# Kernel optimization log

Hardware: AMD Instinct MI355X
Metric: run time of the kernel (lower is better)

The kernel has to match this reference:

```python
import jax, jax.numpy as jnp
import numpy as np

WIN = 3  # win_size from init


def setup_inputs() -> dict:
    key = jax.random.key(0)
    ks = jax.random.split(key, 7)
    B, H, W, d = 8, 128, 128, 128
    N = H * W
    s = d ** -0.5  # param init scale
    return {
        "x": jax.random.normal(ks[0], (B, N, d), dtype=jnp.float32),
        "Wq": jax.random.normal(ks[1], (d, d), dtype=jnp.float32) * s,
        "bq": jax.random.normal(ks[2], (d,), dtype=jnp.float32) * 0.01,
        "Wk": jax.random.normal(ks[3], (d, d), dtype=jnp.float32) * s,
        "bk": jax.random.normal(ks[4], (d,), dtype=jnp.float32) * 0.01,
        "Wv": jax.random.normal(ks[5], (d, d), dtype=jnp.float32) * s,
        "bv": jax.random.normal(ks[6], (d,), dtype=jnp.float32) * 0.01,
        "H": H,
        "W": W,
    }


def reference(x, Wq, bq, Wk, bk, Wv, bv, H, W):
    B, N, d = x.shape
    scale = d ** -0.5
    pad = WIN // 2

    q = (x @ Wq + bq).reshape(B, H, W, d)
    k = (x @ Wk + bk).reshape(B, H, W, d)
    v = (x @ Wv + bv).reshape(B, H, W, d)

    # zero-pad spatial dims (matches F.pad); padded neighbors get logit 0, not -inf
    k_pad = jnp.pad(k, ((0, 0), (pad, pad), (pad, pad), (0, 0)))
    v_pad = jnp.pad(v, ((0, 0), (pad, pad), (pad, pad), (0, 0)))

    scores_l, vs_l = [], []
    for dy in range(WIN):
        for dx in range(WIN):
            k_slice = k_pad[:, dy:dy + H, dx:dx + W]   # [B,H,W,d]
            v_slice = v_pad[:, dy:dy + H, dx:dx + W]
            scores_l.append(jnp.einsum("bhwd,bhwd->bhw", q, k_slice) * scale)
            vs_l.append(v_slice)

    scores = jnp.stack(scores_l, axis=-1)            # [B,H,W,9]
    prob = jax.nn.softmax(scores, axis=-1)           # [B,H,W,9]
    v_stk = jnp.stack(vs_l, axis=-1)                 # [B,H,W,d,9]
    out = jnp.einsum("bhwn,bhwdn->bhwd", prob, v_stk)
    return out.reshape(B, N, d)
```

## Files before the change

kernel.cpp:

```cpp
#include <hip/hip_runtime.h>
#include <stdint.h>

#define B_ 8
#define H_ 128
#define W_ 128
#define D_ 128
#define N_ (H_*W_)
#define M_ (B_*N_)

typedef __attribute__((ext_vector_type(8))) short short8;
typedef __attribute__((ext_vector_type(4))) float floatx4;

typedef const __attribute__((address_space(1))) void* gas_t;
typedef __attribute__((address_space(3))) void* las_t;

__device__ inline unsigned short f2bf(float f){
  union { float f; unsigned int i; } c; c.f = f;
  unsigned int x = c.i;
  x += 0x7FFF + ((x >> 16) & 1);
  return (unsigned short)(x >> 16);
}
__device__ inline float bflo(unsigned int u){
  union { unsigned int i; float f; } c; c.i = u << 16; return c.f;
}
__device__ inline float bfhi(unsigned int u){
  union { unsigned int i; float f; } c; c.i = u & 0xFFFF0000u; return c.f;
}

__global__ void wtrans_kernel(const float* __restrict__ Wq, const float* __restrict__ Wk,
                              const float* __restrict__ Wv, unsigned short* __restrict__ Wt){
  const float* src = blockIdx.x == 0 ? Wq : (blockIdx.x == 1 ? Wk : Wv);
  unsigned short* dst = Wt + blockIdx.x * (D_*D_);
  const int i = blockIdx.y * 256 + threadIdx.x;
  const int k = i >> 7, n = i & 127;
  dst[n*D_ + k] = f2bf(src[i]);
}

__global__ __launch_bounds__(256, 2) void qkv_gemm_kernel(
    const float* __restrict__ x, const unsigned short* __restrict__ Wt,
    const float* __restrict__ bq, const float* __restrict__ bk, const float* __restrict__ bv,
    unsigned short* __restrict__ Q, unsigned short* __restrict__ K, unsigned short* __restrict__ V)
{
  const int which = blockIdx.x;
  const int rowTile = blockIdx.y;
  const float* bias = which == 0 ? bq : (which == 1 ? bk : bv);
  unsigned short* Out = which == 0 ? Q : (which == 1 ? K : V);
  const unsigned short* Wsel = Wt + which * (D_*D_);

  __shared__ unsigned short lds[32768];

  const int t = threadIdx.x;
  const int wave = t >> 6, lane = t & 63;

  {
    #pragma unroll
    for (int p = 0; p < 8; ++p){
      int s = p*256 + t;
      int n = s >> 4, cp = s & 15, c = cp ^ (n & 7);
      const unsigned short* gp = Wsel + n*128 + c*8;
      unsigned short* lp = (unsigned short*)lds + 16384 + p*2048 + wave*512;
      __builtin_amdgcn_global_load_lds((gas_t)(const void*)gp, (las_t)(void*)lp, 16, 0, 0);
    }
  }
  {
    const float* xrow = x + (size_t)rowTile * 128 * D_;
    #pragma unroll
    for (int p = 0; p < 8; ++p){
      int s = p*256 + t;
      int r = s >> 4, cp = s & 15, c = cp ^ (r & 7);
      const float* gp = xrow + r*D_ + c*8;
      float4 f0 = *(const float4*)gp;
      float4 f1 = *(const float4*)(gp + 4);
      uint4 pk;
      pk.x = (unsigned)f2bf(f0.x) | ((unsigned)f2bf(f0.y) << 16);
      pk.y = (unsigned)f2bf(f0.z) | ((unsigned)f2bf(f0.w) << 16);
      pk.z = (unsigned)f2bf(f1.x) | ((unsigned)f2bf(f1.y) << 16);
      pk.w = (unsigned)f2bf(f1.z) | ((unsigned)f2bf(f1.w) << 16);
      *(uint4*)&lds[s*8] = pk;
    }
  }
  __syncthreads();

  const int wm = (wave >> 1) * 64, wn = (wave & 1) * 64;
  const int m0 = lane & 15, quad = lane >> 4;

  floatx4 acc[4][4] = {};
  #pragma unroll
  for (int kk = 0; kk < 4; ++kk){
    short8 a[4], b[4];
    #pragma unroll
    for (int i = 0; i < 4; ++i){
      int row = wm + i*16 + m0;
      int c = (kk*4 + quad) ^ (row & 7);
      a[i] = *(const short8*)&lds[row*128 + c*8];
    }
    #pragma unroll
    for (int j = 0; j < 4; ++j){
      int n = wn + j*16 + m0;
      int c = (kk*4 + quad) ^ (n & 7);
      b[j] = *(const short8*)&lds[16384 + n*128 + c*8];
    }
    #pragma unroll
    for (int i = 0; i < 4; ++i)
      #pragma unroll
      for (int j = 0; j < 4; ++j)
        acc[i][j] = __builtin_amdgcn_mfma_f32_16x16x32_bf16(a[i], b[j], acc[i][j], 0, 0, 0);
  }

  __syncthreads();
  #pragma unroll
  for (int j = 0; j < 4; ++j){
    const int col = wn + j*16 + m0;
    const float bb = bias[col];
    #pragma unroll
    for (int i = 0; i < 4; ++i){
      #pragma unroll
      for (int r = 0; r < 4; ++r){
        int row = wm + i*16 + quad*4 + r;
        lds[row*136 + col] = f2bf(acc[i][j][r] + bb);
      }
    }
  }
  __syncthreads();
  unsigned short* Outp = Out + (size_t)rowTile * 128 * D_;
  #pragma unroll
  for (int p = 0; p < 8; ++p){
    int rr = p*16 + (t >> 4), cc = t & 15;
    uint4 v = *(const uint4*)&lds[rr*136 + cc*8];
    *(uint4*)(Outp + p*2048 + t*8) = v;
  }
}

__global__ __launch_bounds__(256) void attn_kernel(
    const unsigned short* __restrict__ Q, const unsigned short* __restrict__ K,
    const unsigned short* __restrict__ V, float* __restrict__ out)
{
  const int t = threadIdx.x;
  const int quarter = t & 3;
  const int pix = blockIdx.x * 64 + (t >> 2);
  const int w = pix & 127;
  const int h = (pix >> 7) & 127;
  const float scale = 0.08838834764831845f;

  const size_t off = (size_t)pix * D_ + quarter * 32;

  float q[32];
  {
    const unsigned short* qp = Q + off;
    #pragma unroll
    for (int c = 0; c < 4; ++c){
      uint4 u = *(const uint4*)(qp + c*8);
      unsigned uu[4] = {u.x, u.y, u.z, u.w};
      #pragma unroll
      for (int e = 0; e < 4; ++e){
        q[c*8 + e*2]     = bflo(uu[e]) * scale;
        q[c*8 + e*2 + 1] = bfhi(uu[e]) * scale;
      }
    }
  }

  float s[9];
  #pragma unroll
  for (int i = 0; i < 9; ++i){
    const int dy = i/3 - 1, dx = i%3 - 1;
    const bool ok = ((unsigned)(h + dy) < 128u) && ((unsigned)(w + dx) < 128u);
    float acc = 0.f;
    if (ok){
      const unsigned short* kp = K + off + (dy*W_ + dx) * D_;
      #pragma unroll
      for (int c = 0; c < 4; ++c){
        uint4 u = *(const uint4*)(kp + c*8);
        unsigned uu[4] = {u.x, u.y, u.z, u.w};
        #pragma unroll
        for (int e = 0; e < 4; ++e){
          acc += q[c*8 + e*2]     * bflo(uu[e]);
          acc += q[c*8 + e*2 + 1] * bfhi(uu[e]);
        }
      }
    }
    s[i] = acc;
  }
  #pragma unroll
  for (int i = 0; i < 9; ++i){
    s[i] += __shfl_xor(s[i], 1, 64);
    s[i] += __shfl_xor(s[i], 2, 64);
  }

  float m = s[0];
  #pragma unroll
  for (int i = 1; i < 9; ++i) m = fmaxf(m, s[i]);
  float p[9]; float l = 0.f;
  #pragma unroll
  for (int i = 0; i < 9; ++i){ p[i] = __expf(s[i] - m); l += p[i]; }
  const float inv = 1.f / l;

  float o[32];
  #pragma unroll
  for (int d = 0; d < 32; ++d) o[d] = 0.f;
  #pragma unroll
  for (int i = 0; i < 9; ++i){
    const int dy = i/3 - 1, dx = i%3 - 1;
    const bool ok = ((unsigned)(h + dy) < 128u) && ((unsigned)(w + dx) < 128u);
    if (ok){
      const float pi = p[i];
      const unsigned short* vp = V + off + (dy*W_ + dx) * D_;
      #pragma unroll
      for (int c = 0; c < 4; ++c){
        uint4 u = *(const uint4*)(vp + c*8);
        unsigned uu[4] = {u.x, u.y, u.z, u.w};
        #pragma unroll
        for (int e = 0; e < 4; ++e){
          o[c*8 + e*2]     += pi * bflo(uu[e]);
          o[c*8 + e*2 + 1] += pi * bfhi(uu[e]);
        }
      }
    }
  }

  float* op = out + off;
  #pragma unroll
  for (int c = 0; c < 8; ++c){
    float4 v4 = make_float4(o[c*4]*inv, o[c*4+1]*inv, o[c*4+2]*inv, o[c*4+3]*inv);
    *(float4*)(op + c*4) = v4;
  }
}

extern "C" void kernel_launch(void* const* d_in, const int* in_sizes, int n_in,
                              void* d_out, int out_size, void* d_ws, size_t ws_size,
                              hipStream_t stream)
{
  const float* x  = (const float*)d_in[0];
  const float* Wq = (const float*)d_in[1];
  const float* bq = (const float*)d_in[2];
  const float* Wk = (const float*)d_in[3];
  const float* bk = (const float*)d_in[4];
  const float* Wv = (const float*)d_in[5];
  const float* bv = (const float*)d_in[6];
  float* out = (float*)d_out;

  char* ws = (char*)d_ws;
  unsigned short* Wt = (unsigned short*)ws;
  unsigned short* Q  = (unsigned short*)(ws + (1<<17));
  unsigned short* K  = (unsigned short*)(ws + (1<<17) + (size_t)M_*D_*2);
  unsigned short* V  = (unsigned short*)(ws + (1<<17) + (size_t)2*M_*D_*2);

  hipLaunchKernelGGL(wtrans_kernel, dim3(3, 64), dim3(256), 0, stream, Wq, Wk, Wv, Wt);
  hipLaunchKernelGGL(qkv_gemm_kernel, dim3(3, M_/128), dim3(256), 0, stream,
                     x, Wt, bq, bk, bv, Q, K, V);
  hipLaunchKernelGGL(attn_kernel, dim3(M_/64), dim3(256), 0, stream, Q, K, V, out);
}
```

Baseline: 222.3 us.

## Reuse converted x tile across Q/K/V in GEMM; batch neighbor loads in attention

The QKV GEMM now launches one block per 128-row tile and loops over the three projections. The fp32 x tile is loaded and converted to bf16 once instead of three times, and the epilogue is staged in two halves to fit LDS. The attention kernel splits each pixel across 8 lanes of 16 channels instead of 4 lanes of 32, and issues all nine K and V neighbor loads up front into registers to raise memory-level parallelism. The trade-off is fewer, longer GEMM blocks with more barriers, and higher register pressure in attention under the new launch bound.

New measurement: 260.4 us. 17.1% more time.

```diff
diff --git a/kernel.cpp b/kernel.cpp
--- a/kernel.cpp
+++ b/kernel.cpp
@@ -41,27 +41,13 @@
     const float* __restrict__ bq, const float* __restrict__ bk, const float* __restrict__ bv,
     unsigned short* __restrict__ Q, unsigned short* __restrict__ K, unsigned short* __restrict__ V)
 {
-  const int which = blockIdx.x;
-  const int rowTile = blockIdx.y;
-  const float* bias = which == 0 ? bq : (which == 1 ? bk : bv);
-  unsigned short* Out = which == 0 ? Q : (which == 1 ? K : V);
-  const unsigned short* Wsel = Wt + which * (D_*D_);
+  const int rowTile = blockIdx.x;
 
   __shared__ unsigned short lds[32768];
 
   const int t = threadIdx.x;
   const int wave = t >> 6, lane = t & 63;
 
-  {
-    #pragma unroll
-    for (int p = 0; p < 8; ++p){
-      int s = p*256 + t;
-      int n = s >> 4, cp = s & 15, c = cp ^ (n & 7);
-      const unsigned short* gp = Wsel + n*128 + c*8;
-      unsigned short* lp = (unsigned short*)lds + 16384 + p*2048 + wave*512;
-      __builtin_amdgcn_global_load_lds((gas_t)(const void*)gp, (las_t)(void*)lp, 16, 0, 0);
-    }
-  }
   {
     const float* xrow = x + (size_t)rowTile * 128 * D_;
     #pragma unroll
@@ -79,147 +65,182 @@
       *(uint4*)&lds[s*8] = pk;
     }
   }
-  __syncthreads();
 
   const int wm = (wave >> 1) * 64, wn = (wave & 1) * 64;
   const int m0 = lane & 15, quad = lane >> 4;
 
-  floatx4 acc[4][4] = {};
-  #pragma unroll
-  for (int kk = 0; kk < 4; ++kk){
-    short8 a[4], b[4];
-    #pragma unroll
-    for (int i = 0; i < 4; ++i){
-      int row = wm + i*16 + m0;
-      int c = (kk*4 + quad) ^ (row & 7);
-      a[i] = *(const short8*)&lds[row*128 + c*8];
-    }
-    #pragma unroll
-    for (int j = 0; j < 4; ++j){
-      int n = wn + j*16 + m0;
-      int c = (kk*4 + quad) ^ (n & 7);
-      b[j] = *(const short8*)&lds[16384 + n*128 + c*8];
-    }
-    #pragma unroll
-    for (int i = 0; i < 4; ++i)
-      #pragma unroll
-      for (int j = 0; j < 4; ++j)
-        acc[i][j] = __builtin_amdgcn_mfma_f32_16x16x32_bf16(a[i], b[j], acc[i][j], 0, 0, 0);
-  }
-
-  __syncthreads();
-  #pragma unroll
-  for (int j = 0; j < 4; ++j){
-    const int col = wn + j*16 + m0;
-    const float bb = bias[col];
-    #pragma unroll
-    for (int i = 0; i < 4; ++i){
-      #pragma unroll
-      for (int r = 0; r < 4; ++r){
-        int row = wm + i*16 + quad*4 + r;
-        lds[row*136 + col] = f2bf(acc[i][j][r] + bb);
-      }
-    }
-  }
-  __syncthreads();
-  unsigned short* Outp = Out + (size_t)rowTile * 128 * D_;
-  #pragma unroll
-  for (int p = 0; p < 8; ++p){
-    int rr = p*16 + (t >> 4), cc = t & 15;
-    uint4 v = *(const uint4*)&lds[rr*136 + cc*8];
-    *(uint4*)(Outp + p*2048 + t*8) = v;
-  }
-}
-
-__global__ __launch_bounds__(256) void attn_kernel(
+  #pragma unroll
+  for (int which = 0; which < 3; ++which){
+    const float* bias = which == 0 ? bq : (which == 1 ? bk : bv);
+    unsigned short* Out = which == 0 ? Q : (which == 1 ? K : V);
+    const unsigned short* Wsel = Wt + which * (D_*D_);
+
+    #pragma unroll
+    for (int p = 0; p < 8; ++p){
+      int s = p*256 + t;
+      int n = s >> 4, cp = s & 15, c = cp ^ (n & 7);
+      const unsigned short* gp = Wsel + n*128 + c*8;
+      unsigned short* lp = (unsigned short*)lds + 16384 + p*2048 + wave*512;
+      __builtin_amdgcn_global_load_lds((gas_t)(const void*)gp, (las_t)(void*)lp, 16, 0, 0);
+    }
+    __syncthreads();
+
+    floatx4 acc[4][4] = {};
+    #pragma unroll
+    for (int kk = 0; kk < 4; ++kk){
+      short8 a[4], b[4];
+      #pragma unroll
+      for (int i = 0; i < 4; ++i){
+        int row = wm + i*16 + m0;
+        int c = (kk*4 + quad) ^ (row & 7);
+        a[i] = *(const short8*)&lds[row*128 + c*8];
+      }
+      #pragma unroll
+      for (int j = 0; j < 4; ++j){
+        int n = wn + j*16 + m0;
+        int c = (kk*4 + quad) ^ (n & 7);
+        b[j] = *(const short8*)&lds[16384 + n*128 + c*8];
+      }
+      #pragma unroll
+      for (int i = 0; i < 4; ++i)
+        #pragma unroll
+        for (int j = 0; j < 4; ++j)
+          acc[i][j] = __builtin_amdgcn_mfma_f32_16x16x32_bf16(a[i], b[j], acc[i][j], 0, 0, 0);
+    }
+
+    __syncthreads();
+    unsigned short* Outp = Out + (size_t)rowTile * 128 * D_;
+    #pragma unroll
+    for (int half = 0; half < 2; ++half){
+      if ((wave >> 1) == half){
+        #pragma unroll
+        for (int j = 0; j < 4; ++j){
+          const int col = wn + j*16 + m0;
+          const float bb = bias[col];
+          #pragma unroll
+          for (int i = 0; i < 4; ++i){
+            #pragma unroll
+            for (int r = 0; r < 4; ++r){
+              int lrow = i*16 + quad*4 + r;
+              lds[16384 + lrow*136 + col] = f2bf(acc[i][j][r] + bb);
+            }
+          }
+        }
+      }
+      __syncthreads();
+      #pragma unroll
+      for (int p = 0; p < 4; ++p){
+        int rr = p*16 + (t >> 4), cc = t & 15;
+        uint4 vv = *(const uint4*)&lds[16384 + rr*136 + cc*8];
+        *(uint4*)(Outp + half*8192 + p*2048 + t*8) = vv;
+      }
+      __syncthreads();
+    }
+  }
+}
+
+__global__ __launch_bounds__(256, 4) void attn_kernel(
     const unsigned short* __restrict__ Q, const unsigned short* __restrict__ K,
     const unsigned short* __restrict__ V, float* __restrict__ out)
 {
   const int t = threadIdx.x;
-  const int quarter = t & 3;
-  const int pix = blockIdx.x * 64 + (t >> 2);
+  const int e8 = t & 7;
+  const int pix = blockIdx.x * 32 + (t >> 3);
   const int w = pix & 127;
   const int h = (pix >> 7) & 127;
   const float scale = 0.08838834764831845f;
 
-  const size_t off = (size_t)pix * D_ + quarter * 32;
-
-  float q[32];
+  const size_t off = (size_t)pix * D_ + e8 * 16;
+
+  float q[16];
   {
     const unsigned short* qp = Q + off;
-    #pragma unroll
-    for (int c = 0; c < 4; ++c){
-      uint4 u = *(const uint4*)(qp + c*8);
-      unsigned uu[4] = {u.x, u.y, u.z, u.w};
-      #pragma unroll
-      for (int e = 0; e < 4; ++e){
-        q[c*8 + e*2]     = bflo(uu[e]) * scale;
-        q[c*8 + e*2 + 1] = bfhi(uu[e]) * scale;
-      }
-    }
-  }
-
-  float s[9];
-  #pragma unroll
-  for (int i = 0; i < 9; ++i){
-    const int dy = i/3 - 1, dx = i%3 - 1;
-    const bool ok = ((unsigned)(h + dy) < 128u) && ((unsigned)(w + dx) < 128u);
-    float acc = 0.f;
-    if (ok){
-      const unsigned short* kp = K + off + (dy*W_ + dx) * D_;
-      #pragma unroll
-      for (int c = 0; c < 4; ++c){
-        uint4 u = *(const uint4*)(kp + c*8);
-        unsigned uu[4] = {u.x, u.y, u.z, u.w};
-        #pragma unroll
-        for (int e = 0; e < 4; ++e){
-          acc += q[c*8 + e*2]     * bflo(uu[e]);
-          acc += q[c*8 + e*2 + 1] * bfhi(uu[e]);
-        }
-      }
-    }
-    s[i] = acc;
-  }
-  #pragma unroll
-  for (int i = 0; i < 9; ++i){
-    s[i] += __shfl_xor(s[i], 1, 64);
-    s[i] += __shfl_xor(s[i], 2, 64);
-  }
-
-  float m = s[0];
-  #pragma unroll
-  for (int i = 1; i < 9; ++i) m = fmaxf(m, s[i]);
-  float p[9]; float l = 0.f;
-  #pragma unroll
-  for (int i = 0; i < 9; ++i){ p[i] = __expf(s[i] - m); l += p[i]; }
-  const float inv = 1.f / l;
-
-  float o[32];
-  #pragma unroll
-  for (int d = 0; d < 32; ++d) o[d] = 0.f;
+    uint4 u0 = *(const uint4*)qp;
+    uint4 u1 = *(const uint4*)(qp + 8);
+    unsigned uu[8] = {u0.x, u0.y, u0.z, u0.w, u1.x, u1.y, u1.z, u1.w};
+    #pragma unroll
+    for (int e = 0; e < 8; ++e){
+      q[e*2]     = bflo(uu[e]) * scale;
+      q[e*2 + 1] = bfhi(uu[e]) * scale;
+    }
+  }
+
+  uint4 ku[9][2];
   #pragma unroll
   for (int i = 0; i < 9; ++i){
     const int dy = i/3 - 1, dx = i%3 - 1;
     const bool ok = ((unsigned)(h + dy) < 128u) && ((unsigned)(w + dx) < 128u);
     if (ok){
-      const float pi = p[i];
+      const unsigned short* kp = K + off + (dy*W_ + dx) * D_;
+      ku[i][0] = *(const uint4*)kp;
+      ku[i][1] = *(const uint4*)(kp + 8);
+    } else {
+      ku[i][0] = make_uint4(0u,0u,0u,0u);
+      ku[i][1] = make_uint4(0u,0u,0u,0u);
+    }
+  }
+
+  float s[9];
+  #pragma unroll
+  for (int i = 0; i < 9; ++i){
+    unsigned uu[8] = {ku[i][0].x, ku[i][0].y, ku[i][0].z, ku[i][0].w,
+                      ku[i][1].x, ku[i][1].y, ku[i][1].z, ku[i][1].w};
+    float acc = 0.f;
+    #pragma unroll
+    for (int e = 0; e < 8; ++e){
+      acc += q[e*2]     * bflo(uu[e]);
+      acc += q[e*2 + 1] * bfhi(uu[e]);
+    }
+    s[i] = acc;
+  }
+  #pragma unroll
+  for (int i = 0; i < 9; ++i){
+    s[i] += __shfl_xor(s[i], 1, 64);
+    s[i] += __shfl_xor(s[i], 2, 64);
+    s[i] += __shfl_xor(s[i], 4, 64);
+  }
+
+  uint4 vu[9][2];
+  #pragma unroll
+  for (int i = 0; i < 9; ++i){
+    const int dy = i/3 - 1, dx = i%3 - 1;
+    const bool ok = ((unsigned)(h + dy) < 128u) && ((unsigned)(w + dx) < 128u);
+    if (ok){
       const unsigned short* vp = V + off + (dy*W_ + dx) * D_;
-      #pragma unroll
-      for (int c = 0; c < 4; ++c){
-        uint4 u = *(const uint4*)(vp + c*8);
-        unsigned uu[4] = {u.x, u.y, u.z, u.w};
-        #pragma unroll
-        for (int e = 0; e < 4; ++e){
-          o[c*8 + e*2]     += pi * bflo(uu[e]);
-          o[c*8 + e*2 + 1] += pi * bfhi(uu[e]);
-        }
-      }
+      vu[i][0] = *(const uint4*)vp;
+      vu[i][1] = *(const uint4*)(vp + 8);
+    } else {
+      vu[i][0] = make_uint4(0u,0u,0u,0u);
+      vu[i][1] = make_uint4(0u,0u,0u,0u);
+    }
+  }
+
+  float m = s[0];
+  #pragma unroll
+  for (int i = 1; i < 9; ++i) m = fmaxf(m, s[i]);
+  float p[9]; float l = 0.f;
+  #pragma unroll
+  for (int i = 0; i < 9; ++i){ p[i] = __expf(s[i] - m); l += p[i]; }
+  const float inv = 1.f / l;
+
+  float o[16];
+  #pragma unroll
+  for (int d = 0; d < 16; ++d) o[d] = 0.f;
+  #pragma unroll
+  for (int i = 0; i < 9; ++i){
+    const float pi = p[i];
+    unsigned uu[8] = {vu[i][0].x, vu[i][0].y, vu[i][0].z, vu[i][0].w,
+                      vu[i][1].x, vu[i][1].y, vu[i][1].z, vu[i][1].w};
+    #pragma unroll
+    for (int e = 0; e < 8; ++e){
+      o[e*2]     += pi * bflo(uu[e]);
+      o[e*2 + 1] += pi * bfhi(uu[e]);
     }
   }
 
   float* op = out + off;
   #pragma unroll
-  for (int c = 0; c < 8; ++c){
+  for (int c = 0; c < 4; ++c){
     float4 v4 = make_float4(o[c*4]*inv, o[c*4+1]*inv, o[c*4+2]*inv, o[c*4+3]*inv);
     *(float4*)(op + c*4) = v4;
   }
@@ -245,7 +266,7 @@
   unsigned short* V  = (unsigned short*)(ws + (1<<17) + (size_t)2*M_*D_*2);
 
   hipLaunchKernelGGL(wtrans_kernel, dim3(3, 64), dim3(256), 0, stream, Wq, Wk, Wv, Wt);
-  hipLaunchKernelGGL(qkv_gemm_kernel, dim3(3, M_/128), dim3(256), 0, stream,
+  hipLaunchKernelGGL(qkv_gemm_kernel, dim3(M_/128), dim3(256), 0, stream,
                      x, Wt, bq, bk, bv, Q, K, V);
-  hipLaunchKernelGGL(attn_kernel, dim3(M_/64), dim3(256), 0, stream, Q, K, V, out);
-}
+  hipLaunchKernelGGL(attn_kernel, dim3(M_/32), dim3(256), 0, stream, Q, K, V, out);
+}
```

## Fuse QKV projection and windowed attention into one spatially tiled kernel

Applied to the files above, without the earlier changes.

Replaces the separate QKV GEMM and attention kernels with one kernel per 16x16 spatial tile. It computes Q for the tile and K for an 18x18 halo tile in LDS, then forms the softmax-weighted sum of x neighbors and applies Wv once, adding the bias scaled by the sum of probabilities (linearity of V). This removes the Q/K/V round trips through global memory. In exchange it recomputes K over the halo and reads x neighbors in fp32 from global memory, runs only 512 large blocks, and adds a bf16 rounding step on the aggregated x.

Result: slower. 238.6 us (+7.3%).

```diff
diff --git a/kernel.cpp b/kernel.cpp
--- a/kernel.cpp
+++ b/kernel.cpp
@@ -36,192 +36,282 @@
   dst[n*D_ + k] = f2bf(src[i]);
 }
 
-__global__ __launch_bounds__(256, 2) void qkv_gemm_kernel(
+__global__ __launch_bounds__(512, 2) void fused_kernel(
     const float* __restrict__ x, const unsigned short* __restrict__ Wt,
     const float* __restrict__ bq, const float* __restrict__ bk, const float* __restrict__ bv,
-    unsigned short* __restrict__ Q, unsigned short* __restrict__ K, unsigned short* __restrict__ V)
+    float* __restrict__ out)
 {
-  const int which = blockIdx.x;
-  const int rowTile = blockIdx.y;
-  const float* bias = which == 0 ? bq : (which == 1 ? bk : bv);
-  unsigned short* Out = which == 0 ? Q : (which == 1 ? K : V);
-  const unsigned short* Wsel = Wt + which * (D_*D_);
-
-  __shared__ unsigned short lds[32768];
-
-  const int t = threadIdx.x;
-  const int wave = t >> 6, lane = t & 63;
-
-  {
-    #pragma unroll
-    for (int p = 0; p < 8; ++p){
-      int s = p*256 + t;
-      int n = s >> 4, cp = s & 15, c = cp ^ (n & 7);
-      const unsigned short* gp = Wsel + n*128 + c*8;
-      unsigned short* lp = (unsigned short*)lds + 16384 + p*2048 + wave*512;
-      __builtin_amdgcn_global_load_lds((gas_t)(const void*)gp, (las_t)(void*)lp, 16, 0, 0);
-    }
-  }
-  {
-    const float* xrow = x + (size_t)rowTile * 128 * D_;
-    #pragma unroll
-    for (int p = 0; p < 8; ++p){
-      int s = p*256 + t;
-      int r = s >> 4, cp = s & 15, c = cp ^ (r & 7);
-      const float* gp = xrow + r*D_ + c*8;
-      float4 f0 = *(const float4*)gp;
-      float4 f1 = *(const float4*)(gp + 4);
-      uint4 pk;
-      pk.x = (unsigned)f2bf(f0.x) | ((unsigned)f2bf(f0.y) << 16);
-      pk.y = (unsigned)f2bf(f0.z) | ((unsigned)f2bf(f0.w) << 16);
-      pk.z = (unsigned)f2bf(f1.x) | ((unsigned)f2bf(f1.y) << 16);
-      pk.w = (unsigned)f2bf(f1.z) | ((unsigned)f2bf(f1.w) << 16);
-      *(uint4*)&lds[s*8] = pk;
-    }
-  }
-  __syncthreads();
-
-  const int wm = (wave >> 1) * 64, wn = (wave & 1) * 64;
-  const int m0 = lane & 15, quad = lane >> 4;
-
-  floatx4 acc[4][4] = {};
-  #pragma unroll
-  for (int kk = 0; kk < 4; ++kk){
-    short8 a[4], b[4];
-    #pragma unroll
-    for (int i = 0; i < 4; ++i){
-      int row = wm + i*16 + m0;
-      int c = (kk*4 + quad) ^ (row & 7);
-      a[i] = *(const short8*)&lds[row*128 + c*8];
-    }
-    #pragma unroll
-    for (int j = 0; j < 4; ++j){
-      int n = wn + j*16 + m0;
-      int c = (kk*4 + quad) ^ (n & 7);
-      b[j] = *(const short8*)&lds[16384 + n*128 + c*8];
-    }
-    #pragma unroll
-    for (int i = 0; i < 4; ++i)
-      #pragma unroll
-      for (int j = 0; j < 4; ++j)
-        acc[i][j] = __builtin_amdgcn_mfma_f32_16x16x32_bf16(a[i], b[j], acc[i][j], 0, 0, 0);
-  }
-
-  __syncthreads();
-  #pragma unroll
-  for (int j = 0; j < 4; ++j){
-    const int col = wn + j*16 + m0;
-    const float bb = bias[col];
-    #pragma unroll
-    for (int i = 0; i < 4; ++i){
-      #pragma unroll
-      for (int r = 0; r < 4; ++r){
-        int row = wm + i*16 + quad*4 + r;
-        lds[row*136 + col] = f2bf(acc[i][j][r] + bb);
-      }
-    }
-  }
-  __syncthreads();
-  unsigned short* Outp = Out + (size_t)rowTile * 128 * D_;
-  #pragma unroll
-  for (int p = 0; p < 8; ++p){
-    int rr = p*16 + (t >> 4), cc = t & 15;
-    uint4 v = *(const uint4*)&lds[rr*136 + cc*8];
-    *(uint4*)(Outp + p*2048 + t*8) = v;
-  }
-}
-
-__global__ __launch_bounds__(256) void attn_kernel(
-    const unsigned short* __restrict__ Q, const unsigned short* __restrict__ K,
-    const unsigned short* __restrict__ V, float* __restrict__ out)
-{
-  const int t = threadIdx.x;
-  const int quarter = t & 3;
-  const int pix = blockIdx.x * 64 + (t >> 2);
-  const int w = pix & 127;
-  const int h = (pix >> 7) & 127;
+  __shared__ unsigned short lds[65536];
+
+  const int u = threadIdx.x;
+  const int wave = u >> 6, lane = u & 63, m0 = lane & 15, quad = lane >> 4;
+  const int tile = blockIdx.x;
+  const int img = tile >> 6, ty = (tile >> 3) & 7, tx = tile & 7;
+  const int h0 = ty*16, w0 = tx*16;
+  const float* xi = x + (size_t)img * N_ * D_;
+  float* outp = out + (size_t)img * N_ * D_;
+  const int px = u >> 1, tq = u & 1;
+  const int ph = px >> 4, pw = px & 15;
   const float scale = 0.08838834764831845f;
 
-  const size_t off = (size_t)pix * D_ + quarter * 32;
-
-  float q[32];
-  {
-    const unsigned short* qp = Q + off;
-    #pragma unroll
-    for (int c = 0; c < 4; ++c){
-      uint4 u = *(const uint4*)(qp + c*8);
-      unsigned uu[4] = {u.x, u.y, u.z, u.w};
-      #pragma unroll
-      for (int e = 0; e < 4; ++e){
-        q[c*8 + e*2]     = bflo(uu[e]) * scale;
-        q[c*8 + e*2 + 1] = bfhi(uu[e]) * scale;
-      }
-    }
-  }
-
-  float s[9];
-  #pragma unroll
-  for (int i = 0; i < 9; ++i){
-    const int dy = i/3 - 1, dx = i%3 - 1;
-    const bool ok = ((unsigned)(h + dy) < 128u) && ((unsigned)(w + dx) < 128u);
-    float acc = 0.f;
-    if (ok){
-      const unsigned short* kp = K + off + (dy*W_ + dx) * D_;
-      #pragma unroll
-      for (int c = 0; c < 4; ++c){
-        uint4 u = *(const uint4*)(kp + c*8);
-        unsigned uu[4] = {u.x, u.y, u.z, u.w};
+  auto stage_W = [&](int which){
+    const unsigned short* Ws = Wt + which*(D_*D_);
+    #pragma unroll
+    for (int p = 0; p < 4; ++p){
+      int s = p*512 + u, n = s >> 4, cp = s & 15, c = cp ^ (n & 7);
+      __builtin_amdgcn_global_load_lds((gas_t)(const void*)(Ws + n*128 + c*8),
+          (las_t)(void*)((unsigned short*)lds + p*4096 + wave*512), 16, 0, 0);
+    }
+  };
+
+  stage_W(0);
+  short8 a[4][2];
+  {
+    float4 f[8][2];
+    #pragma unroll
+    for (int i = 0; i < 2; ++i)
+      #pragma unroll
+      for (int kk = 0; kk < 4; ++kk){
+        const float* gp = xi + (size_t)((h0 + wave*2 + i)*W_ + w0 + m0)*D_ + kk*32 + quad*8;
+        f[i*4+kk][0] = *(const float4*)gp;
+        f[i*4+kk][1] = *(const float4*)(gp + 4);
+      }
+    __builtin_amdgcn_sched_barrier(0);
+    #pragma unroll
+    for (int i = 0; i < 2; ++i)
+      #pragma unroll
+      for (int kk = 0; kk < 4; ++kk){
+        short8 v;
+        v[0]=(short)f2bf(f[i*4+kk][0].x); v[1]=(short)f2bf(f[i*4+kk][0].y);
+        v[2]=(short)f2bf(f[i*4+kk][0].z); v[3]=(short)f2bf(f[i*4+kk][0].w);
+        v[4]=(short)f2bf(f[i*4+kk][1].x); v[5]=(short)f2bf(f[i*4+kk][1].y);
+        v[6]=(short)f2bf(f[i*4+kk][1].z); v[7]=(short)f2bf(f[i*4+kk][1].w);
+        a[kk][i] = v;
+      }
+  }
+  __syncthreads();
+
+  {
+    floatx4 acc[8][2] = {};
+    #pragma unroll
+    for (int kk = 0; kk < 4; ++kk){
+      #pragma unroll
+      for (int j = 0; j < 8; ++j){
+        int n = j*16 + m0;
+        int c = (kk*4 + quad) ^ (n & 7);
+        short8 b = *(const short8*)&lds[n*128 + c*8];
+        #pragma unroll
+        for (int i = 0; i < 2; ++i)
+          acc[j][i] = __builtin_amdgcn_mfma_f32_16x16x32_bf16(b, a[kk][i], acc[j][i], 0, 0, 0);
+      }
+    }
+    #pragma unroll
+    for (int j = 0; j < 8; ++j){
+      const float4 bb = *(const float4*)&bq[j*16 + quad*4];
+      #pragma unroll
+      for (int i = 0; i < 2; ++i){
+        int row = wave*32 + i*16 + m0;
+        int chunk = j*2 + (quad >> 1);
+        uint2 pk;
+        pk.x = (unsigned)f2bf(acc[j][i][0]+bb.x) | ((unsigned)f2bf(acc[j][i][1]+bb.y) << 16);
+        pk.y = (unsigned)f2bf(acc[j][i][2]+bb.z) | ((unsigned)f2bf(acc[j][i][3]+bb.w) << 16);
+        *(uint2*)&lds[16384 + row*128 + ((chunk ^ (row & 7)) << 3) + ((quad & 1) << 2)] = pk;
+      }
+    }
+  }
+  __syncthreads();
+
+  uint4 qb[8];
+  #pragma unroll
+  for (int c = 0; c < 8; ++c){
+    int chunk = tq*8 + c;
+    qb[c] = *(const uint4*)&lds[16384 + px*128 + ((chunk ^ (px & 7)) << 3)];
+  }
+  stage_W(1);
+  short8 ak[4][3];
+  {
+    int grh[3];
+    #pragma unroll
+    for (int i = 0; i < 3; ++i){
+      int hp = wave*48 + i*16 + m0;
+      int hy = hp / 18, hx = hp - hy*18;
+      int th = h0 - 1 + hy, tw = w0 - 1 + hx;
+      th = min(max(th, 0), 127); tw = min(max(tw, 0), 127);
+      grh[i] = th*W_ + tw;
+    }
+    #pragma unroll
+    for (int i = 0; i < 3; ++i){
+      float4 g[4][2];
+      #pragma unroll
+      for (int kk = 0; kk < 4; ++kk){
+        const float* gp = xi + (size_t)grh[i]*D_ + kk*32 + quad*8;
+        g[kk][0] = *(const float4*)gp;
+        g[kk][1] = *(const float4*)(gp + 4);
+      }
+      __builtin_amdgcn_sched_barrier(0);
+      #pragma unroll
+      for (int kk = 0; kk < 4; ++kk){
+        short8 v;
+        v[0]=(short)f2bf(g[kk][0].x); v[1]=(short)f2bf(g[kk][0].y);
+        v[2]=(short)f2bf(g[kk][0].z); v[3]=(short)f2bf(g[kk][0].w);
+        v[4]=(short)f2bf(g[kk][1].x); v[5]=(short)f2bf(g[kk][1].y);
+        v[6]=(short)f2bf(g[kk][1].z); v[7]=(short)f2bf(g[kk][1].w);
+        ak[kk][i] = v;
+      }
+    }
+  }
+  __syncthreads();
+
+  {
+    floatx4 acc[8][3] = {};
+    #pragma unroll
+    for (int kk = 0; kk < 4; ++kk){
+      #pragma unroll
+      for (int j = 0; j < 8; ++j){
+        int n = j*16 + m0;
+        int c = (kk*4 + quad) ^ (n & 7);
+        short8 b = *(const short8*)&lds[n*128 + c*8];
+        #pragma unroll
+        for (int i = 0; i < 3; ++i)
+          acc[j][i] = __builtin_amdgcn_mfma_f32_16x16x32_bf16(b, ak[kk][i], acc[j][i], 0, 0, 0);
+      }
+    }
+    #pragma unroll
+    for (int j = 0; j < 8; ++j){
+      const float4 bb = *(const float4*)&bk[j*16 + quad*4];
+      #pragma unroll
+      for (int i = 0; i < 3; ++i){
+        int row = wave*48 + i*16 + m0;
+        int chunk = j*2 + (quad >> 1);
+        uint2 pk;
+        pk.x = (unsigned)f2bf(acc[j][i][0]+bb.x) | ((unsigned)f2bf(acc[j][i][1]+bb.y) << 16);
+        pk.y = (unsigned)f2bf(acc[j][i][2]+bb.z) | ((unsigned)f2bf(acc[j][i][3]+bb.w) << 16);
+        *(uint2*)&lds[16384 + row*128 + ((chunk ^ (row & 7)) << 3) + ((quad & 1) << 2)] = pk;
+      }
+    }
+  }
+  __syncthreads();
+
+  stage_W(2);
+  float qf[64];
+  #pragma unroll
+  for (int c = 0; c < 8; ++c){
+    unsigned uu[4] = {qb[c].x, qb[c].y, qb[c].z, qb[c].w};
+    #pragma unroll
+    for (int e = 0; e < 4; ++e){
+      qf[c*8 + e*2]     = bflo(uu[e]) * scale;
+      qf[c*8 + e*2 + 1] = bfhi(uu[e]) * scale;
+    }
+  }
+  float pim[9]; int gr9[9];
+  {
+    float s[9];
+    #pragma unroll
+    for (int i9 = 0; i9 < 9; ++i9){
+      const int di = i9/3 - 1, dj = i9%3 - 1;
+      const int hidx = (ph + 1 + di)*18 + (pw + 1 + dj);
+      float acc = 0.f;
+      #pragma unroll
+      for (int c = 0; c < 8; ++c){
+        int chunk = tq*8 + c;
+        uint4 kv = *(const uint4*)&lds[16384 + hidx*128 + ((chunk ^ (hidx & 7)) << 3)];
+        unsigned uu[4] = {kv.x, kv.y, kv.z, kv.w};
         #pragma unroll
         for (int e = 0; e < 4; ++e){
-          acc += q[c*8 + e*2]     * bflo(uu[e]);
-          acc += q[c*8 + e*2 + 1] * bfhi(uu[e]);
+          acc += qf[c*8 + e*2]     * bflo(uu[e]);
+          acc += qf[c*8 + e*2 + 1] * bfhi(uu[e]);
         }
       }
-    }
-    s[i] = acc;
-  }
-  #pragma unroll
-  for (int i = 0; i < 9; ++i){
-    s[i] += __shfl_xor(s[i], 1, 64);
-    s[i] += __shfl_xor(s[i], 2, 64);
-  }
-
-  float m = s[0];
-  #pragma unroll
-  for (int i = 1; i < 9; ++i) m = fmaxf(m, s[i]);
-  float p[9]; float l = 0.f;
-  #pragma unroll
-  for (int i = 0; i < 9; ++i){ p[i] = __expf(s[i] - m); l += p[i]; }
-  const float inv = 1.f / l;
-
-  float o[32];
-  #pragma unroll
-  for (int d = 0; d < 32; ++d) o[d] = 0.f;
-  #pragma unroll
-  for (int i = 0; i < 9; ++i){
-    const int dy = i/3 - 1, dx = i%3 - 1;
-    const bool ok = ((unsigned)(h + dy) < 128u) && ((unsigned)(w + dx) < 128u);
-    if (ok){
-      const float pi = p[i];
-      const unsigned short* vp = V + off + (dy*W_ + dx) * D_;
-      #pragma unroll
-      for (int c = 0; c < 4; ++c){
-        uint4 u = *(const uint4*)(vp + c*8);
-        unsigned uu[4] = {u.x, u.y, u.z, u.w};
+      acc += __shfl_xor(acc, 1, 64);
+      const int th = h0 + ph + di, tw = w0 + pw + dj;
+      const bool ok = ((unsigned)th < 128u) && ((unsigned)tw < 128u);
+      s[i9] = ok ? acc : 0.f;
+      const int ch = min(max(th, 0), 127), cw = min(max(tw, 0), 127);
+      gr9[i9] = ch*W_ + cw;
+      pim[i9] = ok ? 1.f : 0.f;
+    }
+    float mx = s[0];
+    #pragma unroll
+    for (int i9 = 1; i9 < 9; ++i9) mx = fmaxf(mx, s[i9]);
+    float l = 0.f;
+    #pragma unroll
+    for (int i9 = 0; i9 < 9; ++i9){ float e = __expf(s[i9] - mx); s[i9] = e; l += e; }
+    const float inv = 1.f / l;
+    #pragma unroll
+    for (int i9 = 0; i9 < 9; ++i9) pim[i9] *= s[i9] * inv;
+  }
+  float sps = 0.f;
+  #pragma unroll
+  for (int i9 = 0; i9 < 9; ++i9) sps += pim[i9];
+  float y[64];
+  #pragma unroll
+  for (int d = 0; d < 64; ++d) y[d] = 0.f;
+  #pragma unroll
+  for (int i9 = 0; i9 < 9; ++i9){
+    const float pi = pim[i9];
+    const float* gp = xi + (size_t)gr9[i9]*D_ + tq*64;
+    #pragma unroll
+    for (int c2 = 0; c2 < 16; ++c2){
+      float4 xv = *(const float4*)(gp + c2*4);
+      y[c2*4+0] += pi*xv.x; y[c2*4+1] += pi*xv.y;
+      y[c2*4+2] += pi*xv.z; y[c2*4+3] += pi*xv.w;
+    }
+  }
+  __syncthreads();
+
+  #pragma unroll
+  for (int c = 0; c < 8; ++c){
+    uint4 pk;
+    pk.x = (unsigned)f2bf(y[c*8+0]) | ((unsigned)f2bf(y[c*8+1]) << 16);
+    pk.y = (unsigned)f2bf(y[c*8+2]) | ((unsigned)f2bf(y[c*8+3]) << 16);
+    pk.z = (unsigned)f2bf(y[c*8+4]) | ((unsigned)f2bf(y[c*8+5]) << 16);
+    pk.w = (unsigned)f2bf(y[c*8+6]) | ((unsigned)f2bf(y[c*8+7]) << 16);
+    int chunk = tq*8 + c;
+    *(uint4*)&lds[16384 + px*128 + ((chunk ^ (px & 7)) << 3)] = pk;
+  }
+  {
+    float* sPw = (float*)&lds[16384 + 380*128];
+    if (tq == 0) sPw[px] = sps;
+  }
+  __syncthreads();
+
+  {
+    short8 ay[4][2];
+    #pragma unroll
+    for (int kk = 0; kk < 4; ++kk)
+      #pragma unroll
+      for (int i = 0; i < 2; ++i){
+        int row = wave*32 + i*16 + m0;
+        int c = (kk*4 + quad) ^ (row & 7);
+        ay[kk][i] = *(const short8*)&lds[16384 + row*128 + c*8];
+      }
+    floatx4 acc[8][2] = {};
+    #pragma unroll
+    for (int kk = 0; kk < 4; ++kk){
+      #pragma unroll
+      for (int j = 0; j < 8; ++j){
+        int n = j*16 + m0;
+        int c = (kk*4 + quad) ^ (n & 7);
+        short8 b = *(const short8*)&lds[n*128 + c*8];
         #pragma unroll
-        for (int e = 0; e < 4; ++e){
-          o[c*8 + e*2]     += pi * bflo(uu[e]);
-          o[c*8 + e*2 + 1] += pi * bfhi(uu[e]);
-        }
-      }
-    }
-  }
-
-  float* op = out + off;
-  #pragma unroll
-  for (int c = 0; c < 8; ++c){
-    float4 v4 = make_float4(o[c*4]*inv, o[c*4+1]*inv, o[c*4+2]*inv, o[c*4+3]*inv);
-    *(float4*)(op + c*4) = v4;
+        for (int i = 0; i < 2; ++i)
+          acc[j][i] = __builtin_amdgcn_mfma_f32_16x16x32_bf16(b, ay[kk][i], acc[j][i], 0, 0, 0);
+      }
+    }
+    const float* sPr = (const float*)&lds[16384 + 380*128];
+    #pragma unroll
+    for (int j = 0; j < 8; ++j){
+      const float4 bb = *(const float4*)&bv[j*16 + quad*4];
+      #pragma unroll
+      for (int i = 0; i < 2; ++i){
+        int row = wave*32 + i*16 + m0;
+        float sp = sPr[row];
+        int gr = (h0 + wave*2 + i)*W_ + w0 + m0;
+        float4 v = make_float4(acc[j][i][0] + sp*bb.x, acc[j][i][1] + sp*bb.y,
+                               acc[j][i][2] + sp*bb.z, acc[j][i][3] + sp*bb.w);
+        *(float4*)(outp + (size_t)gr*D_ + j*16 + quad*4) = v;
+      }
+    }
   }
 }
 
@@ -238,14 +328,9 @@
   const float* bv = (const float*)d_in[6];
   float* out = (float*)d_out;
 
-  char* ws = (char*)d_ws;
-  unsigned short* Wt = (unsigned short*)ws;
-  unsigned short* Q  = (unsigned short*)(ws + (1<<17));
-  unsigned short* K  = (unsigned short*)(ws + (1<<17) + (size_t)M_*D_*2);
-  unsigned short* V  = (unsigned short*)(ws + (1<<17) + (size_t)2*M_*D_*2);
+  unsigned short* Wt = (unsigned short*)d_ws;
 
   hipLaunchKernelGGL(wtrans_kernel, dim3(3, 64), dim3(256), 0, stream, Wq, Wk, Wv, Wt);
-  hipLaunchKernelGGL(qkv_gemm_kernel, dim3(3, M_/128), dim3(256), 0, stream,
-                     x, Wt, bq, bk, bv, Q, K, V);
-  hipLaunchKernelGGL(attn_kernel, dim3(M_/64), dim3(256), 0, stream, Q, K, V, out);
-}
+  hipLaunchKernelGGL(fused_kernel, dim3(512), dim3(512), 0, stream,
+                     x, Wt, bq, bk, bv, out);
+}
```
